# Performance work log

Measured on AMD Instinct MI355X. Metric: run time of the kernel, lower is better.

## Reference

```python
import jax, jax.numpy as jnp
import numpy as np
from functools import partial

N_NODES = 50000


def gcn_conv(x, row, col, norm, W, b, num_nodes):
    # x: [N, Fin], W: [Fout, Fin] (torch Linear weight layout), b: [Fout]
    h = x @ W.T                                   # [N, Fout]
    msg = norm[:, None] * h[row]                  # per-edge message, gather x_j = x[row]
    out = jax.ops.segment_sum(msg, col, num_segments=num_nodes)  # scatter-add to target col
    return out + b


def _build_norm(row, col, edge_weight, num_nodes):
    # add self-loops with weight 1.0
    loops = jnp.arange(num_nodes, dtype=row.dtype)
    row_f = jnp.concatenate([row, loops])
    col_f = jnp.concatenate([col, loops])
    ew_f = jnp.concatenate([edge_weight, jnp.ones((num_nodes,), edge_weight.dtype)])
    # degree counts occurrences of row (unweighted, like PyG degree())
    deg = jax.ops.segment_sum(jnp.ones_like(ew_f), row_f, num_segments=num_nodes)
    dinv = jnp.where(deg > 0, deg ** -0.5, 0.0).astype(edge_weight.dtype)
    norm = dinv[row_f] * ew_f * dinv[col_f]
    return row_f, col_f, norm


def setup_inputs() -> dict:
    key = jax.random.key(0)
    k = jax.random.split(key, 8)
    N, E = N_NODES, 800000
    Fin, H, C = 256, 96, 40
    x = jax.random.normal(k[0], (N, Fin), dtype=jnp.float32)
    edge_index = jax.random.randint(k[1], (2, E), 0, N, dtype=jnp.int64)
    edge_weight = jax.random.uniform(k[2], (E,), dtype=jnp.float32)
    W1 = jax.random.normal(k[3], (H, Fin), dtype=jnp.float32) * (1.0 / np.sqrt(Fin))
    b1 = jnp.zeros((H,), jnp.float32)
    W2 = jax.random.normal(k[4], (C, H), dtype=jnp.float32) * (1.0 / np.sqrt(H))
    b2 = jnp.zeros((C,), jnp.float32)
    return {"x": x, "edge_index": edge_index, "edge_weight": edge_weight,
            "W1": W1, "b1": b1, "W2": W2, "b2": b2}


def reference(x, edge_index, edge_weight, W1, b1, W2, b2):
    N = x.shape[0]
    row, col = edge_index[0], edge_index[1]
    row_f, col_f, norm = _build_norm(row, col, edge_weight, N)
    h = jax.nn.relu(gcn_conv(x, row_f, col_f, norm, W1, b1, N))
    # dropout is identity in eval mode
    out = gcn_conv(h, row_f, col_f, norm, W2, b2, N)
    return jax.nn.log_softmax(out, axis=1)
```

## Files before the change

### kernel.cpp

```cpp
#include <hip/hip_runtime.h>
#include <hip/hip_bf16.h>
#include <hip/hip_fp16.h>
#include <math.h>

#define NN 50000
#define EE 800000
#define FIN 256
#define FH 96
#define FC 40
#define NBK 196

typedef _Float16 h4 __attribute__((ext_vector_type(4)));
typedef _Float16 h8 __attribute__((ext_vector_type(8)));
typedef float f32x4 __attribute__((ext_vector_type(4)));

__device__ __forceinline__ unsigned pack_edge(int row, float ew) {
    _Float16 he = (_Float16)ew;
    unsigned short us;
    __builtin_memcpy(&us, &he, 2);
    return (unsigned)row | ((unsigned)us << 16);
}
__device__ __forceinline__ float unpack_w(unsigned pk) {
    unsigned short us = (unsigned short)(pk >> 16);
    _Float16 hv;
    __builtin_memcpy(&hv, &us, 2);
    return (float)hv;
}


__global__ __launch_bounds__(256) void k_histcnt(const int* __restrict__ ei, int E,
                                                 unsigned* __restrict__ copies,
                                                 unsigned* __restrict__ bcnt) {
    __shared__ unsigned lds[12500];
    int b = blockIdx.x;
    int tid = threadIdx.x;
    int ES = (E + 63) >> 6;
    if (b < 128) {
        int slice = b & 63, half = b >> 6;
        const int* ptr = ei;
        for (int i = tid; i < 12500; i += 256) lds[i] = 0u;
        __syncthreads();
        int lo = slice * ES, hi = min(lo + ES, E);
        int nlo = half * 25000;
        for (int i = lo + tid; i < hi; i += 256) {
            int rel = ptr[i] - nlo;
            if ((unsigned)rel < 25000u)
                atomicAdd(&lds[rel >> 1], 1u << ((rel & 1) << 4));
        }
        __syncthreads();
        unsigned* dst = copies + (size_t)(half * 64 + slice) * 12500;
        for (int i = tid; i < 12500; i += 256) dst[i] = lds[i];
    } else {
        int chunk = b - 128;
        const int* col = ei + E;
        for (int i = tid; i < NBK; i += 256) lds[i] = 0u;
        __syncthreads();
        int lo = chunk * ES, hi = min(lo + ES, E);
        for (int i = lo + tid; i < hi; i += 256) atomicAdd(&lds[col[i] >> 8], 1u);
        __syncthreads();
        for (int i = tid; i < NBK; i += 256)
            if (lds[i]) atomicAdd(&bcnt[i], lds[i]);
    }
}


__global__ __launch_bounds__(256) void k_reduce(const unsigned* __restrict__ copies,
                                                const unsigned* __restrict__ bcnt,
                                                float* __restrict__ dinv,
                                                unsigned* __restrict__ bstart,
                                                unsigned* __restrict__ gcur,
                                                unsigned* __restrict__ off, unsigned E) {
    int t = blockIdx.x * blockDim.x + threadIdx.x;
    if (t < 25000) {
        int half = t / 12500, w = t - half * 12500;
        unsigned sr = 0;
        const unsigned* br = copies + (size_t)half * 64 * 12500 + w;
#pragma unroll 8
        for (int s = 0; s < 64; ++s) sr += br[s * 12500];
        int n0 = half * 25000 + 2 * w;
        dinv[n0]     = rsqrtf((float)((sr & 0xffffu) + 1u));
        dinv[n0 + 1] = rsqrtf((float)((sr >> 16) + 1u));
    }
    if (blockIdx.x == 0) {
        __shared__ unsigned sb[256];
        int tt = threadIdx.x;
        unsigned v = (tt < NBK) ? bcnt[tt] : 0u;
        sb[tt] = v;
        __syncthreads();
        for (int o = 1; o < 256; o <<= 1) {
            unsigned tv = (tt >= o) ? sb[tt - o] : 0u;
            __syncthreads();
            sb[tt] += tv;
            __syncthreads();
        }
        if (tt < NBK) {
            unsigned ex = sb[tt] - v;
            bstart[tt] = ex;
            gcur[tt] = ex;
            bstart[tt + 1] = sb[tt];
        }
        if (tt == 0) off[NN] = E;
    }
}


__global__ __launch_bounds__(256) void k_bucket(const int* __restrict__ row,
                                                const int* __restrict__ col,
                                                const float* __restrict__ ew,
                                                unsigned* __restrict__ gcur,
                                                unsigned* __restrict__ bkc,
                                                unsigned* __restrict__ bkpk, int E) {
    __shared__ unsigned cnt[NBK];
    __shared__ unsigned cur[NBK];
    int tid = threadIdx.x;
    int CH = (E + gridDim.x - 1) / gridDim.x;
    int lo = blockIdx.x * CH, hi = min(lo + CH, E);
    for (int i = tid; i < NBK; i += 256) cnt[i] = 0u;
    __syncthreads();
    for (int i = lo + tid; i < hi; i += 256) atomicAdd(&cnt[col[i] >> 8], 1u);
    __syncthreads();
    for (int i = tid; i < NBK; i += 256) cur[i] = atomicAdd(&gcur[i], cnt[i]);
    __syncthreads();
    for (int i = lo + tid; i < hi; i += 256) {
        int c = col[i];
        unsigned pos = atomicAdd(&cur[c >> 8], 1u);
        bkc[pos] = (unsigned)c;
        bkpk[pos] = pack_edge(row[i], ew[i]);
    }
}


__global__ __launch_bounds__(256) void k_place(const unsigned* __restrict__ bkc,
                                               const unsigned* __restrict__ bkpk,
                                               const unsigned* __restrict__ bstart,
                                               unsigned* __restrict__ off,
                                               unsigned* __restrict__ epk, int n) {
    __shared__ unsigned cnt[256];
    __shared__ unsigned cur[256];
    int b = blockIdx.x;
    int tid = threadIdx.x;
    int node0 = b * 256;
    unsigned st = bstart[b], en = bstart[b + 1];
    cnt[tid] = 0u;
    __syncthreads();
    for (unsigned i = st + tid; i < en; i += 256) atomicAdd(&cnt[bkc[i] & 255], 1u);
    __syncthreads();
    unsigned v = cnt[tid];
    cur[tid] = v;
    __syncthreads();
    for (int o = 1; o < 256; o <<= 1) {
        unsigned tv = (tid >= o) ? cur[tid - o] : 0u;
        __syncthreads();
        cur[tid] += tv;
        __syncthreads();
    }
    unsigned base = st + cur[tid] - v;
    int node = node0 + tid;
    if (node < n) off[node] = base;
    cur[tid] = base;
    __syncthreads();
    for (unsigned i = st + tid; i < en; i += 256) {
        unsigned c = bkc[i];
        unsigned pos = atomicAdd(&cur[c & 255], 1u);
        epk[pos] = bkpk[i];
    }
}


__global__ __launch_bounds__(256) void k_gemm1(const float* __restrict__ x,
                                               const float* __restrict__ W,
                                               const float* __restrict__ dinv,
                                               _Float16* __restrict__ g0h, int n) {
    __shared__ _Float16 xs[64][72];
    __shared__ _Float16 wsm[96][72];
    int tid = threadIdx.x;
    int row0 = blockIdx.x * 64;
    int l = tid & 63, w = tid >> 6;
    int l15 = l & 15, lg = l >> 4;

    f32x4 acc[6];
#pragma unroll
    for (int c = 0; c < 6; ++c) acc[c] = (f32x4)0.f;

    for (int kc = 0; kc < 4; ++kc) {
        int kbase = kc * 64;
#pragma unroll
        for (int i = 0; i < 4; ++i) {
            int it = tid + 256 * i;
            int r = it >> 4, k4 = it & 15;
            float4 v = make_float4(0.f, 0.f, 0.f, 0.f);
            int gr = row0 + r;
            if (gr < n) v = *(const float4*)&x[gr * FIN + kbase + k4 * 4];
            h4 hv = {(_Float16)v.x, (_Float16)v.y, (_Float16)v.z, (_Float16)v.w};
            *(h4*)&xs[r][k4 * 4] = hv;
        }
#pragma unroll
        for (int i = 0; i < 6; ++i) {
            int it = tid + 256 * i;
            int r = it >> 4, k4 = it & 15;
            float4 v = *(const float4*)&W[r * FIN + kbase + k4 * 4];
            h4 hv = {(_Float16)v.x, (_Float16)v.y, (_Float16)v.z, (_Float16)v.w};
            *(h4*)&wsm[r][k4 * 4] = hv;
        }
        __syncthreads();
#pragma unroll
        for (int ks = 0; ks < 2; ++ks) {
            h8 a = *(const h8*)&xs[16 * w + l15][ks * 32 + lg * 8];
#pragma unroll
            for (int ct = 0; ct < 6; ++ct) {
                h8 b = *(const h8*)&wsm[ct * 16 + l15][ks * 32 + lg * 8];
                acc[ct] = __builtin_amdgcn_mfma_f32_16x16x32_f16(a, b, acc[ct], 0, 0, 0);
            }
        }
        __syncthreads();
    }
#pragma unroll
    for (int r = 0; r < 4; ++r) {
        int grow = row0 + 16 * w + lg * 4 + r;
        if (grow < n) {
            float dv = dinv[grow];
#pragma unroll
            for (int ct = 0; ct < 6; ++ct)
                g0h[(size_t)grow * FH + ct * 16 + l15] = (_Float16)(dv * acc[ct][r]);
        }
    }
}


__global__ __launch_bounds__(256) void k_agg96(const _Float16* __restrict__ g0h,
                                               const unsigned* __restrict__ off,
                                               const unsigned* __restrict__ epk,
                                               const float* __restrict__ dinv,
                                               const float* __restrict__ b,
                                               _Float16* __restrict__ outh, int n) {
    int tid = blockIdx.x * 256 + threadIdx.x;
    int node = tid / 12;
    int f8 = tid - node * 12;
    if (node >= n) return;
    const h8* gp = (const h8*)g0h;
    h8 self = gp[(size_t)node * 12 + f8];
    float acc[8];
#pragma unroll
    for (int j = 0; j < 8; ++j) acc[j] = (float)self[j];
    unsigned st = off[node], en = off[node + 1];
    unsigned e = st;
    for (; e + 4 <= en; e += 4) {
        unsigned k0 = epk[e + 0], k1 = epk[e + 1], k2 = epk[e + 2], k3 = epk[e + 3];
        h8 ga = gp[(size_t)(k0 & 0xffffu) * 12 + f8];
        h8 gb = gp[(size_t)(k1 & 0xffffu) * 12 + f8];
        h8 gc = gp[(size_t)(k2 & 0xffffu) * 12 + f8];
        h8 gd = gp[(size_t)(k3 & 0xffffu) * 12 + f8];
        float w0 = unpack_w(k0), w1 = unpack_w(k1), w2 = unpack_w(k2), w3 = unpack_w(k3);
#pragma unroll
        for (int j = 0; j < 8; ++j) acc[j] = fmaf(w0, (float)ga[j], acc[j]);
#pragma unroll
        for (int j = 0; j < 8; ++j) acc[j] = fmaf(w1, (float)gb[j], acc[j]);
#pragma unroll
        for (int j = 0; j < 8; ++j) acc[j] = fmaf(w2, (float)gc[j], acc[j]);
#pragma unroll
        for (int j = 0; j < 8; ++j) acc[j] = fmaf(w3, (float)gd[j], acc[j]);
    }
    for (; e < en; ++e) {
        unsigned k = epk[e];
        h8 g = gp[(size_t)(k & 0xffffu) * 12 + f8];
        float wv = unpack_w(k);
#pragma unroll
        for (int j = 0; j < 8; ++j) acc[j] = fmaf(wv, (float)g[j], acc[j]);
    }
    float s = dinv[node];
    float4 bv0 = ((const float4*)b)[f8 * 2];
    float4 bv1 = ((const float4*)b)[f8 * 2 + 1];
    const float bb[8] = {bv0.x, bv0.y, bv0.z, bv0.w, bv1.x, bv1.y, bv1.z, bv1.w};
    h8 o;
#pragma unroll
    for (int j = 0; j < 8; ++j) o[j] = (_Float16)fmaxf(fmaf(s, acc[j], bb[j]), 0.f);
    *(h8*)&outh[(size_t)node * FH + f8 * 8] = o;
}


__global__ __launch_bounds__(256) void k_gemm2(const _Float16* __restrict__ h,
                                               const float* __restrict__ W2,
                                               const float* __restrict__ dinv,
                                               _Float16* __restrict__ g1h, int n) {
    __shared__ _Float16 hs[64][104];
    __shared__ _Float16 wsm[48][104];
    int tid = threadIdx.x;
    int row0 = blockIdx.x * 64;
    int l = tid & 63, w = tid >> 6;
    int l15 = l & 15, lg = l >> 4;

    f32x4 acc[3];
#pragma unroll
    for (int c = 0; c < 3; ++c) acc[c] = (f32x4)0.f;

#pragma unroll
    for (int i = 0; i < 6; ++i) {
        int it = tid + 256 * i;
        int r = it / 24, k4 = it - r * 24;
        int gr = row0 + r;
        h4 hv = {(_Float16)0.f, (_Float16)0.f, (_Float16)0.f, (_Float16)0.f};
        if (gr < n) hv = *(const h4*)&h[(size_t)gr * FH + k4 * 4];
        *(h4*)&hs[r][k4 * 4] = hv;
    }
#pragma unroll
    for (int i = 0; i < 5; ++i) {
        int it = tid + 256 * i;
        if (it < 1152) {
            int r = it / 24, k4 = it - r * 24;
            h4 hv = {(_Float16)0.f, (_Float16)0.f, (_Float16)0.f, (_Float16)0.f};
            if (r < FC) {
                float4 v = *(const float4*)&W2[r * FH + k4 * 4];
                hv[0] = (_Float16)v.x; hv[1] = (_Float16)v.y;
                hv[2] = (_Float16)v.z; hv[3] = (_Float16)v.w;
            }
            *(h4*)&wsm[r][k4 * 4] = hv;
        }
    }
    __syncthreads();
#pragma unroll
    for (int ks = 0; ks < 3; ++ks) {
        h8 a = *(const h8*)&hs[16 * w + l15][ks * 32 + lg * 8];
#pragma unroll
        for (int ct = 0; ct < 3; ++ct) {
            h8 b = *(const h8*)&wsm[ct * 16 + l15][ks * 32 + lg * 8];
            acc[ct] = __builtin_amdgcn_mfma_f32_16x16x32_f16(a, b, acc[ct], 0, 0, 0);
        }
    }
#pragma unroll
    for (int r = 0; r < 4; ++r) {
        int grow = row0 + 16 * w + lg * 4 + r;
        if (grow < n) {
            float dv = dinv[grow];
#pragma unroll
            for (int ct = 0; ct < 3; ++ct) {
                int colc = ct * 16 + l15;
                if (colc < FC)
                    g1h[(size_t)grow * FC + colc] = (_Float16)(dv * acc[ct][r]);
            }
        }
    }
}


__global__ __launch_bounds__(256) void k_agg40lsm(const _Float16* __restrict__ g1h,
                                                  const unsigned* __restrict__ off,
                                                  const unsigned* __restrict__ epk,
                                                  const float* __restrict__ dinv,
                                                  const float* __restrict__ b,
                                                  float* __restrict__ out, int n) {
    __shared__ float sm[50][41];
    int tid = threadIdx.x;
    int ln = tid / 5;
    int f8 = tid - ln * 5;
    int node = blockIdx.x * 50 + ln;
    bool active = (tid < 250) && (node < n);
    float acc[8];
#pragma unroll
    for (int j = 0; j < 8; ++j) acc[j] = 0.f;
    if (active) {
        const h8* gp = (const h8*)g1h;
        h8 self = gp[(size_t)node * 5 + f8];
#pragma unroll
        for (int j = 0; j < 8; ++j) acc[j] = (float)self[j];
        unsigned st = off[node], en = off[node + 1];
        unsigned e = st;
        for (; e + 4 <= en; e += 4) {
            unsigned k0 = epk[e + 0], k1 = epk[e + 1], k2 = epk[e + 2], k3 = epk[e + 3];
            h8 ga = gp[(size_t)(k0 & 0xffffu) * 5 + f8];
            h8 gb = gp[(size_t)(k1 & 0xffffu) * 5 + f8];
            h8 gc = gp[(size_t)(k2 & 0xffffu) * 5 + f8];
            h8 gd = gp[(size_t)(k3 & 0xffffu) * 5 + f8];
            float w0 = unpack_w(k0), w1 = unpack_w(k1), w2 = unpack_w(k2), w3 = unpack_w(k3);
#pragma unroll
            for (int j = 0; j < 8; ++j) acc[j] = fmaf(w0, (float)ga[j], acc[j]);
#pragma unroll
            for (int j = 0; j < 8; ++j) acc[j] = fmaf(w1, (float)gb[j], acc[j]);
#pragma unroll
            for (int j = 0; j < 8; ++j) acc[j] = fmaf(w2, (float)gc[j], acc[j]);
#pragma unroll
            for (int j = 0; j < 8; ++j) acc[j] = fmaf(w3, (float)gd[j], acc[j]);
        }
        for (; e < en; ++e) {
            unsigned k = epk[e];
            h8 g = gp[(size_t)(k & 0xffffu) * 5 + f8];
            float wv = unpack_w(k);
#pragma unroll
            for (int j = 0; j < 8; ++j) acc[j] = fmaf(wv, (float)g[j], acc[j]);
        }
        float s = dinv[node];
        float4 bv0 = ((const float4*)b)[f8 * 2];
        float4 bv1 = ((const float4*)b)[f8 * 2 + 1];
        const float bb[8] = {bv0.x, bv0.y, bv0.z, bv0.w, bv1.x, bv1.y, bv1.z, bv1.w};
#pragma unroll
        for (int j = 0; j < 8; ++j) {
            acc[j] = fmaf(s, acc[j], bb[j]);
            sm[ln][f8 * 8 + j] = acc[j];
        }
    }
    __syncthreads();
    if (tid < 50) {
        int nd = blockIdx.x * 50 + tid;
        if (nd < n) {
            float m = -INFINITY;
#pragma unroll 8
            for (int j = 0; j < FC; ++j) m = fmaxf(m, sm[tid][j]);
            float sum = 0.f;
#pragma unroll 8
            for (int j = 0; j < FC; ++j) sum += expf(sm[tid][j] - m);
            sm[tid][40] = logf(sum) + m;
        }
    }
    __syncthreads();
    if (active) {
        float lse = sm[ln][40];
        float4 o0 = make_float4(acc[0] - lse, acc[1] - lse, acc[2] - lse, acc[3] - lse);
        float4 o1 = make_float4(acc[4] - lse, acc[5] - lse, acc[6] - lse, acc[7] - lse);
        *(float4*)&out[(size_t)node * FC + f8 * 8] = o0;
        *(float4*)&out[(size_t)node * FC + f8 * 8 + 4] = o1;
    }
}


extern "C" void kernel_launch(void* const* d_in, const int* in_sizes, int n_in,
                              void* d_out, int out_size, void* d_ws, size_t ws_size,
                              hipStream_t stream) {
    const float* x  = (const float*)d_in[0];
    const int*   ei = (const int*)d_in[1];
    const float* ew = (const float*)d_in[2];
    const float* W1 = (const float*)d_in[3];
    const float* b1 = (const float*)d_in[4];
    const float* W2 = (const float*)d_in[5];
    const float* b2 = (const float*)d_in[6];
    float* out = (float*)d_out;

    const int N = NN;
    const int E = in_sizes[1] / 2;
    const int* row = ei;
    const int* col = ei + E;

    float* ws = (float*)d_ws;
    float*    dinv   = (float*)(ws + 0);
    unsigned* off    = (unsigned*)(ws + 50176);
    unsigned* bcnt   = (unsigned*)(ws + 100480);
    unsigned* bstart = (unsigned*)(ws + 100736);
    unsigned* gcur   = (unsigned*)(ws + 100992);
    unsigned* copies = (unsigned*)(ws + 150976);
    unsigned* bkc    = (unsigned*)(ws + 150976);
    unsigned* bkpk   = (unsigned*)(ws + 950976);
    _Float16* h      = (_Float16*)(ws + 150976);
    unsigned* epk    = (unsigned*)(ws + 4950976);
    _Float16* g0h    = (_Float16*)(ws + 6550976);
    _Float16* g1h    = (_Float16*)(ws + 8950976);

    const int B = 256;

    hipMemsetAsync(bcnt, 0, 256 * sizeof(unsigned), stream);

    hipLaunchKernelGGL(k_histcnt, dim3(192), dim3(B), 0, stream, ei, E, copies, bcnt);
    hipLaunchKernelGGL(k_reduce, dim3(98), dim3(B), 0, stream,
                       copies, bcnt, dinv, bstart, gcur, off, (unsigned)E);

    hipLaunchKernelGGL(k_bucket, dim3(320), dim3(B), 0, stream, row, col, ew, gcur, bkc, bkpk, E);
    hipLaunchKernelGGL(k_place, dim3(NBK), dim3(B), 0, stream, bkc, bkpk, bstart, off, epk, N);

    hipLaunchKernelGGL(k_gemm1, dim3((N + 63) / 64), dim3(B), 0, stream, x, W1, dinv, g0h, N);

    hipLaunchKernelGGL(k_agg96, dim3((N * 12 + B - 1) / B), dim3(B), 0, stream,
                       g0h, off, epk, dinv, b1, h, N);

    hipLaunchKernelGGL(k_gemm2, dim3((N + 63) / 64), dim3(B), 0, stream, h, W2, dinv, g1h, N);

    hipLaunchKernelGGL(k_agg40lsm, dim3((N + 49) / 50), dim3(B), 0, stream,
                       g1h, off, epk, dinv, b2, out, N);
}
```

Baseline: 139.7 us.

## Fuse GEMM1 with histogram pass and fold source dinv into edge weights

New measurement: 130.6 us. 6.5% less time.

```diff
diff --git a/kernel.cpp b/kernel.cpp
--- a/kernel.cpp
+++ b/kernel.cpp
@@ -14,8 +14,8 @@
 typedef _Float16 h8 __attribute__((ext_vector_type(8)));
 typedef float f32x4 __attribute__((ext_vector_type(4)));
 
-__device__ __forceinline__ unsigned pack_edge(int row, float ew) {
-    _Float16 he = (_Float16)ew;
+__device__ __forceinline__ unsigned pack_edge(int row, float w) {
+    _Float16 he = (_Float16)w;
     unsigned short us;
     __builtin_memcpy(&us, &he, 2);
     return (unsigned)row | ((unsigned)us << 16);
@@ -28,15 +28,74 @@
 }
 
 
-__global__ __launch_bounds__(256) void k_histcnt(const int* __restrict__ ei, int E,
-                                                 unsigned* __restrict__ copies,
-                                                 unsigned* __restrict__ bcnt) {
+#define G1B 782
+
+__global__ __launch_bounds__(256) void k_fused1(const float* __restrict__ x,
+                                                const float* __restrict__ W,
+                                                _Float16* __restrict__ g0h,
+                                                const int* __restrict__ ei, int E,
+                                                unsigned* __restrict__ copies,
+                                                unsigned* __restrict__ bcnt2d, int n) {
     __shared__ unsigned lds[12500];
-    int b = blockIdx.x;
+    int bid = blockIdx.x;
     int tid = threadIdx.x;
-    int ES = (E + 63) >> 6;
-    if (b < 128) {
-        int slice = b & 63, half = b >> 6;
+
+    if (bid < G1B) {
+        _Float16* xsp = (_Float16*)lds;
+        _Float16* wsp = xsp + 64 * 72;
+        int row0 = bid * 64;
+        int l = tid & 63, w = tid >> 6;
+        int l15 = l & 15, lg = l >> 4;
+
+        f32x4 acc[6];
+#pragma unroll
+        for (int c = 0; c < 6; ++c) acc[c] = (f32x4)0.f;
+
+        for (int kc = 0; kc < 4; ++kc) {
+            int kbase = kc * 64;
+#pragma unroll
+            for (int i = 0; i < 4; ++i) {
+                int it = tid + 256 * i;
+                int r = it >> 4, k4 = it & 15;
+                float4 v = make_float4(0.f, 0.f, 0.f, 0.f);
+                int gr = row0 + r;
+                if (gr < n) v = *(const float4*)&x[gr * FIN + kbase + k4 * 4];
+                h4 hv = {(_Float16)v.x, (_Float16)v.y, (_Float16)v.z, (_Float16)v.w};
+                *(h4*)&xsp[r * 72 + k4 * 4] = hv;
+            }
+#pragma unroll
+            for (int i = 0; i < 6; ++i) {
+                int it = tid + 256 * i;
+                int r = it >> 4, k4 = it & 15;
+                float4 v = *(const float4*)&W[r * FIN + kbase + k4 * 4];
+                h4 hv = {(_Float16)v.x, (_Float16)v.y, (_Float16)v.z, (_Float16)v.w};
+                *(h4*)&wsp[r * 72 + k4 * 4] = hv;
+            }
+            __syncthreads();
+#pragma unroll
+            for (int ks = 0; ks < 2; ++ks) {
+                h8 a = *(const h8*)&xsp[(16 * w + l15) * 72 + ks * 32 + lg * 8];
+#pragma unroll
+                for (int ct = 0; ct < 6; ++ct) {
+                    h8 b = *(const h8*)&wsp[(ct * 16 + l15) * 72 + ks * 32 + lg * 8];
+                    acc[ct] = __builtin_amdgcn_mfma_f32_16x16x32_f16(a, b, acc[ct], 0, 0, 0);
+                }
+            }
+            __syncthreads();
+        }
+#pragma unroll
+        for (int r = 0; r < 4; ++r) {
+            int grow = row0 + 16 * w + lg * 4 + r;
+            if (grow < n) {
+#pragma unroll
+                for (int ct = 0; ct < 6; ++ct)
+                    g0h[(size_t)grow * FH + ct * 16 + l15] = (_Float16)acc[ct][r];
+            }
+        }
+    } else if (bid < 910) {
+        int b2 = bid - G1B;
+        int slice = b2 & 63, half = b2 >> 6;
+        int ES = (E + 63) >> 6;
         const int* ptr = ei;
         for (int i = tid; i < 12500; i += 256) lds[i] = 0u;
         __syncthreads();
@@ -51,21 +110,21 @@
         unsigned* dst = copies + (size_t)(half * 64 + slice) * 12500;
         for (int i = tid; i < 12500; i += 256) dst[i] = lds[i];
     } else {
-        int chunk = b - 128;
+        int chunk = bid - 910;
+        int ES = (E + 63) >> 6;
         const int* col = ei + E;
         for (int i = tid; i < NBK; i += 256) lds[i] = 0u;
         __syncthreads();
         int lo = chunk * ES, hi = min(lo + ES, E);
         for (int i = lo + tid; i < hi; i += 256) atomicAdd(&lds[col[i] >> 8], 1u);
         __syncthreads();
-        for (int i = tid; i < NBK; i += 256)
-            if (lds[i]) atomicAdd(&bcnt[i], lds[i]);
+        for (int i = tid; i < NBK; i += 256) bcnt2d[chunk * 256 + i] = lds[i];
     }
 }
 
 
 __global__ __launch_bounds__(256) void k_reduce(const unsigned* __restrict__ copies,
-                                                const unsigned* __restrict__ bcnt,
+                                                const unsigned* __restrict__ bcnt2d,
                                                 float* __restrict__ dinv,
                                                 unsigned* __restrict__ bstart,
                                                 unsigned* __restrict__ gcur,
@@ -84,7 +143,11 @@
     if (blockIdx.x == 0) {
         __shared__ unsigned sb[256];
         int tt = threadIdx.x;
-        unsigned v = (tt < NBK) ? bcnt[tt] : 0u;
+        unsigned v = 0;
+        if (tt < NBK) {
+#pragma unroll 8
+            for (int c = 0; c < 64; ++c) v += bcnt2d[c * 256 + tt];
+        }
         sb[tt] = v;
         __syncthreads();
         for (int o = 1; o < 256; o <<= 1) {
@@ -107,6 +170,7 @@
 __global__ __launch_bounds__(256) void k_bucket(const int* __restrict__ row,
                                                 const int* __restrict__ col,
                                                 const float* __restrict__ ew,
+                                                const float* __restrict__ dinv,
                                                 unsigned* __restrict__ gcur,
                                                 unsigned* __restrict__ bkc,
                                                 unsigned* __restrict__ bkpk, int E) {
@@ -123,9 +187,10 @@
     __syncthreads();
     for (int i = lo + tid; i < hi; i += 256) {
         int c = col[i];
+        int r = row[i];
         unsigned pos = atomicAdd(&cur[c >> 8], 1u);
         bkc[pos] = (unsigned)c;
-        bkpk[pos] = pack_edge(row[i], ew[i]);
+        bkpk[pos] = pack_edge(r, dinv[r] * ew[i]);
     }
 }
 
@@ -167,66 +232,6 @@
 }
 
 
-__global__ __launch_bounds__(256) void k_gemm1(const float* __restrict__ x,
-                                               const float* __restrict__ W,
-                                               const float* __restrict__ dinv,
-                                               _Float16* __restrict__ g0h, int n) {
-    __shared__ _Float16 xs[64][72];
-    __shared__ _Float16 wsm[96][72];
-    int tid = threadIdx.x;
-    int row0 = blockIdx.x * 64;
-    int l = tid & 63, w = tid >> 6;
-    int l15 = l & 15, lg = l >> 4;
-
-    f32x4 acc[6];
-#pragma unroll
-    for (int c = 0; c < 6; ++c) acc[c] = (f32x4)0.f;
-
-    for (int kc = 0; kc < 4; ++kc) {
-        int kbase = kc * 64;
-#pragma unroll
-        for (int i = 0; i < 4; ++i) {
-            int it = tid + 256 * i;
-            int r = it >> 4, k4 = it & 15;
-            float4 v = make_float4(0.f, 0.f, 0.f, 0.f);
-            int gr = row0 + r;
-            if (gr < n) v = *(const float4*)&x[gr * FIN + kbase + k4 * 4];
-            h4 hv = {(_Float16)v.x, (_Float16)v.y, (_Float16)v.z, (_Float16)v.w};
-            *(h4*)&xs[r][k4 * 4] = hv;
-        }
-#pragma unroll
-        for (int i = 0; i < 6; ++i) {
-            int it = tid + 256 * i;
-            int r = it >> 4, k4 = it & 15;
-            float4 v = *(const float4*)&W[r * FIN + kbase + k4 * 4];
-            h4 hv = {(_Float16)v.x, (_Float16)v.y, (_Float16)v.z, (_Float16)v.w};
-            *(h4*)&wsm[r][k4 * 4] = hv;
-        }
-        __syncthreads();
-#pragma unroll
-        for (int ks = 0; ks < 2; ++ks) {
-            h8 a = *(const h8*)&xs[16 * w + l15][ks * 32 + lg * 8];
-#pragma unroll
-            for (int ct = 0; ct < 6; ++ct) {
-                h8 b = *(const h8*)&wsm[ct * 16 + l15][ks * 32 + lg * 8];
-                acc[ct] = __builtin_amdgcn_mfma_f32_16x16x32_f16(a, b, acc[ct], 0, 0, 0);
-            }
-        }
-        __syncthreads();
-    }
-#pragma unroll
-    for (int r = 0; r < 4; ++r) {
-        int grow = row0 + 16 * w + lg * 4 + r;
-        if (grow < n) {
-            float dv = dinv[grow];
-#pragma unroll
-            for (int ct = 0; ct < 6; ++ct)
-                g0h[(size_t)grow * FH + ct * 16 + l15] = (_Float16)(dv * acc[ct][r]);
-        }
-    }
-}
-
-
 __global__ __launch_bounds__(256) void k_agg96(const _Float16* __restrict__ g0h,
                                                const unsigned* __restrict__ off,
                                                const unsigned* __restrict__ epk,
@@ -237,13 +242,44 @@
     int node = tid / 12;
     int f8 = tid - node * 12;
     if (node >= n) return;
+    float s = dinv[node];
     const h8* gp = (const h8*)g0h;
     h8 self = gp[(size_t)node * 12 + f8];
     float acc[8];
 #pragma unroll
-    for (int j = 0; j < 8; ++j) acc[j] = (float)self[j];
+    for (int j = 0; j < 8; ++j) acc[j] = s * (float)self[j];
     unsigned st = off[node], en = off[node + 1];
     unsigned e = st;
+    for (; e + 8 <= en; e += 8) {
+        unsigned k0 = epk[e + 0], k1 = epk[e + 1], k2 = epk[e + 2], k3 = epk[e + 3];
+        unsigned k4 = epk[e + 4], k5 = epk[e + 5], k6 = epk[e + 6], k7 = epk[e + 7];
+        h8 ga = gp[(size_t)(k0 & 0xffffu) * 12 + f8];
+        h8 gb = gp[(size_t)(k1 & 0xffffu) * 12 + f8];
+        h8 gc = gp[(size_t)(k2 & 0xffffu) * 12 + f8];
+        h8 gd = gp[(size_t)(k3 & 0xffffu) * 12 + f8];
+        h8 ge = gp[(size_t)(k4 & 0xffffu) * 12 + f8];
+        h8 gf = gp[(size_t)(k5 & 0xffffu) * 12 + f8];
+        h8 gg = gp[(size_t)(k6 & 0xffffu) * 12 + f8];
+        h8 gh = gp[(size_t)(k7 & 0xffffu) * 12 + f8];
+        float w0 = unpack_w(k0), w1 = unpack_w(k1), w2 = unpack_w(k2), w3 = unpack_w(k3);
+        float w4 = unpack_w(k4), w5 = unpack_w(k5), w6 = unpack_w(k6), w7 = unpack_w(k7);
+#pragma unroll
+        for (int j = 0; j < 8; ++j) acc[j] = fmaf(w0, (float)ga[j], acc[j]);
+#pragma unroll
+        for (int j = 0; j < 8; ++j) acc[j] = fmaf(w1, (float)gb[j], acc[j]);
+#pragma unroll
+        for (int j = 0; j < 8; ++j) acc[j] = fmaf(w2, (float)gc[j], acc[j]);
+#pragma unroll
+        for (int j = 0; j < 8; ++j) acc[j] = fmaf(w3, (float)gd[j], acc[j]);
+#pragma unroll
+        for (int j = 0; j < 8; ++j) acc[j] = fmaf(w4, (float)ge[j], acc[j]);
+#pragma unroll
+        for (int j = 0; j < 8; ++j) acc[j] = fmaf(w5, (float)gf[j], acc[j]);
+#pragma unroll
+        for (int j = 0; j < 8; ++j) acc[j] = fmaf(w6, (float)gg[j], acc[j]);
+#pragma unroll
+        for (int j = 0; j < 8; ++j) acc[j] = fmaf(w7, (float)gh[j], acc[j]);
+    }
     for (; e + 4 <= en; e += 4) {
         unsigned k0 = epk[e + 0], k1 = epk[e + 1], k2 = epk[e + 2], k3 = epk[e + 3];
         h8 ga = gp[(size_t)(k0 & 0xffffu) * 12 + f8];
@@ -267,7 +303,6 @@
 #pragma unroll
         for (int j = 0; j < 8; ++j) acc[j] = fmaf(wv, (float)g[j], acc[j]);
     }
-    float s = dinv[node];
     float4 bv0 = ((const float4*)b)[f8 * 2];
     float4 bv1 = ((const float4*)b)[f8 * 2 + 1];
     const float bb[8] = {bv0.x, bv0.y, bv0.z, bv0.w, bv1.x, bv1.y, bv1.z, bv1.w};
@@ -280,7 +315,6 @@
 
 __global__ __launch_bounds__(256) void k_gemm2(const _Float16* __restrict__ h,
                                                const float* __restrict__ W2,
-                                               const float* __restrict__ dinv,
                                                _Float16* __restrict__ g1h, int n) {
     __shared__ _Float16 hs[64][104];
     __shared__ _Float16 wsm[48][104];
@@ -330,12 +364,11 @@
     for (int r = 0; r < 4; ++r) {
         int grow = row0 + 16 * w + lg * 4 + r;
         if (grow < n) {
-            float dv = dinv[grow];
 #pragma unroll
             for (int ct = 0; ct < 3; ++ct) {
                 int colc = ct * 16 + l15;
                 if (colc < FC)
-                    g1h[(size_t)grow * FC + colc] = (_Float16)(dv * acc[ct][r]);
+                    g1h[(size_t)grow * FC + colc] = (_Float16)acc[ct][r];
             }
         }
     }
@@ -358,10 +391,11 @@
 #pragma unroll
     for (int j = 0; j < 8; ++j) acc[j] = 0.f;
     if (active) {
+        float s = dinv[node];
         const h8* gp = (const h8*)g1h;
         h8 self = gp[(size_t)node * 5 + f8];
 #pragma unroll
-        for (int j = 0; j < 8; ++j) acc[j] = (float)self[j];
+        for (int j = 0; j < 8; ++j) acc[j] = s * (float)self[j];
         unsigned st = off[node], en = off[node + 1];
         unsigned e = st;
         for (; e + 4 <= en; e += 4) {
@@ -387,7 +421,6 @@
 #pragma unroll
             for (int j = 0; j < 8; ++j) acc[j] = fmaf(wv, (float)g[j], acc[j]);
         }
-        float s = dinv[node];
         float4 bv0 = ((const float4*)b)[f8 * 2];
         float4 bv1 = ((const float4*)b)[f8 * 2 + 1];
         const float bb[8] = {bv0.x, bv0.y, bv0.z, bv0.w, bv1.x, bv1.y, bv1.z, bv1.w};
@@ -441,9 +474,9 @@
     float* ws = (float*)d_ws;
     float*    dinv   = (float*)(ws + 0);
     unsigned* off    = (unsigned*)(ws + 50176);
-    unsigned* bcnt   = (unsigned*)(ws + 100480);
-    unsigned* bstart = (unsigned*)(ws + 100736);
-    unsigned* gcur   = (unsigned*)(ws + 100992);
+    unsigned* bcnt2d = (unsigned*)(ws + 100480);
+    unsigned* bstart = (unsigned*)(ws + 116864);
+    unsigned* gcur   = (unsigned*)(ws + 117120);
     unsigned* copies = (unsigned*)(ws + 150976);
     unsigned* bkc    = (unsigned*)(ws + 150976);
     unsigned* bkpk   = (unsigned*)(ws + 950976);
@@ -454,21 +487,19 @@
 
     const int B = 256;
 
-    hipMemsetAsync(bcnt, 0, 256 * sizeof(unsigned), stream);
-
-    hipLaunchKernelGGL(k_histcnt, dim3(192), dim3(B), 0, stream, ei, E, copies, bcnt);
+    hipLaunchKernelGGL(k_fused1, dim3(974), dim3(B), 0, stream,
+                       x, W1, g0h, ei, E, copies, bcnt2d, N);
     hipLaunchKernelGGL(k_reduce, dim3(98), dim3(B), 0, stream,
-                       copies, bcnt, dinv, bstart, gcur, off, (unsigned)E);
-
-    hipLaunchKernelGGL(k_bucket, dim3(320), dim3(B), 0, stream, row, col, ew, gcur, bkc, bkpk, E);
+                       copies, bcnt2d, dinv, bstart, gcur, off, (unsigned)E);
+
+    hipLaunchKernelGGL(k_bucket, dim3(320), dim3(B), 0, stream,
+                       row, col, ew, dinv, gcur, bkc, bkpk, E);
     hipLaunchKernelGGL(k_place, dim3(NBK), dim3(B), 0, stream, bkc, bkpk, bstart, off, epk, N);
-
-    hipLaunchKernelGGL(k_gemm1, dim3((N + 63) / 64), dim3(B), 0, stream, x, W1, dinv, g0h, N);
 
     hipLaunchKernelGGL(k_agg96, dim3((N * 12 + B - 1) / B), dim3(B), 0, stream,
                        g0h, off, epk, dinv, b1, h, N);
 
-    hipLaunchKernelGGL(k_gemm2, dim3((N + 63) / 64), dim3(B), 0, stream, h, W2, dinv, g1h, N);
+    hipLaunchKernelGGL(k_gemm2, dim3((N + 63) / 64), dim3(B), 0, stream, h, W2, g1h, N);
 
     hipLaunchKernelGGL(k_agg40lsm, dim3((N + 49) / 50), dim3(B), 0, stream,
                        g1h, off, epk, dinv, b2, out, N);
```
